# Performance work log

Hardware: AMD Instinct MI355X
Metric: run time of the kernel (lower is better)

The kernel has to match this reference:

```python
import jax, jax.numpy as jnp
import numpy as np

WL_IDX = 0          # water_level_index
THRESH = 0.1        # anomaly threshold
B, T, I, H, O = 2048, 2048, 8, 24, 1


def setup_inputs() -> dict:
    key = jax.random.key(0)
    ks = jax.random.split(key, 7)
    s = float(1.0 / np.sqrt(H))  # PyTorch LSTMCell/Linear uniform init bound
    x = jax.random.normal(ks[0], (B, T, I), dtype=jnp.float32)
    W_ih = jax.random.uniform(ks[1], (4 * H, I), minval=-s, maxval=s, dtype=jnp.float32)
    W_hh = jax.random.uniform(ks[2], (4 * H, H), minval=-s, maxval=s, dtype=jnp.float32)
    b_ih = jax.random.uniform(ks[3], (4 * H,), minval=-s, maxval=s, dtype=jnp.float32)
    b_hh = jax.random.uniform(ks[4], (4 * H,), minval=-s, maxval=s, dtype=jnp.float32)
    W_out = jax.random.uniform(ks[5], (O, H), minval=-s, maxval=s, dtype=jnp.float32)
    b_out = jax.random.uniform(ks[6], (O,), minval=-s, maxval=s, dtype=jnp.float32)
    return {"x": x, "W_ih": W_ih, "W_hh": W_hh, "b_ih": b_ih, "b_hh": b_hh,
            "W_out": W_out, "b_out": b_out}


def reference(x, W_ih, W_hh, b_ih, b_hh, W_out, b_out):
    # x: (B, T, I) -> preds: (B, T, O)
    Bs, Ts, Is = x.shape
    Hs = W_hh.shape[1]
    h0 = jnp.zeros((Bs, Hs), x.dtype)
    c0 = jnp.zeros((Bs, Hs), x.dtype)
    # Init pred equal to t=0 water level -> anomaly flag is False at t=0,
    # reproducing the original's ungated first step.
    pred0 = x[:, 0, WL_IDX:WL_IDX + 1]  # (B, 1)
    xs = jnp.swapaxes(x, 0, 1)  # (T, B, I)

    def step(carry, x_t):
        h, c, pred = carry
        actual = x_t[:, WL_IDX:WL_IDX + 1]            # (B, 1)
        anom = jnp.abs(pred - actual) > THRESH         # (B, 1) bool
        wl = jnp.where(anom[:, 0], pred[:, 0], x_t[:, WL_IDX])
        inp = x_t.at[:, WL_IDX].set(wl)                # anomaly-gated input
        # LSTMCell: gates in PyTorch order i, f, g, o
        gates = inp @ W_ih.T + b_ih + h @ W_hh.T + b_hh  # (B, 4H)
        i_g, f_g, g_g, o_g = jnp.split(gates, 4, axis=1)
        c_new = jax.nn.sigmoid(f_g) * c + jax.nn.sigmoid(i_g) * jnp.tanh(g_g)
        h_new = jax.nn.sigmoid(o_g) * jnp.tanh(c_new)
        pred_new = h_new @ W_out.T + b_out             # (B, O)
        return (h_new, c_new, pred_new), pred_new

    _, preds = jax.lax.scan(step, (h0, c0, pred0), xs)  # (T, B, O)
    return jnp.swapaxes(preds, 0, 1)  # (B, T, O)
```

## Files before the change

kernel.cpp:

```cpp
#include <hip/hip_runtime.h>

#define TT 2048
#define II 8
#define HH 24
#define THRESH 0.1f
#define LOG2E 1.4426950408889634f

typedef float v2f __attribute__((ext_vector_type(2)));

#define ROR_ADD(a, N)                                                          \
    {                                                                          \
        int t_ = __builtin_amdgcn_update_dpp(0, __float_as_int(a),             \
                                             0x120 + (N), 0xF, 0xF, false);    \
        (a) += __int_as_float(t_);                                             \
    }

__global__ __launch_bounds__(64)
__attribute__((amdgpu_waves_per_eu(2, 2)))
void lstm_anom_kernel(const float* __restrict__ x,
                      const float* __restrict__ W_ih,
                      const float* __restrict__ W_hh,
                      const float* __restrict__ b_ih,
                      const float* __restrict__ b_hh,
                      const float* __restrict__ W_out,
                      const float* __restrict__ b_out,
                      float* __restrict__ out)
{
    __shared__ __align__(16) float vbuf[32];

    const int  lane  = threadIdx.x;
    const int  b     = blockIdx.x;
    const int  l32   = lane & 31;
    const bool hi    = lane >= 32;
    const bool unitL = (l32 < HH);
    const int  jc    = unitL ? l32 : 0;
    const bool xL    = (!hi) && (l32 >= 24);
    const int  xk    = l32 - 24;

    const float* xb = x + (size_t)b * (TT * II);

    const int rowA = (hi ? 2 * HH : 0) + jc;
    const int rowB = rowA + HH;
    volatile const float* vW_ih = W_ih;
    volatile const float* vW_hh = W_hh;

    v2f wA2[16], wB2[16];
    #pragma unroll
    for (int k = 0; k < 4; ++k) {
        wA2[k] = (v2f){ vW_ih[rowA * II + 2 * k], vW_ih[rowA * II + 2 * k + 1] };
        wB2[k] = (v2f){ vW_ih[rowB * II + 2 * k], vW_ih[rowB * II + 2 * k + 1] };
    }
    #pragma unroll
    for (int k = 0; k < 12; ++k) {
        wA2[4 + k] = (v2f){ vW_hh[rowA * HH + 2 * k], vW_hh[rowA * HH + 2 * k + 1] };
        wB2[4 + k] = (v2f){ vW_hh[rowB * HH + 2 * k], vW_hh[rowB * HH + 2 * k + 1] };
    }
    const float biasA = b_ih[rowA] + b_hh[rowA];
    const float biasB = b_ih[rowB] + b_hh[rowB];
    const float kA = hi ? (-2.f * LOG2E) : (-LOG2E);
    const float mA = hi ? 2.f : 1.f;
    const float nA = hi ? -1.f : 0.f;
    const float woutj = unitL ? W_out[jc] : 0.f;
    const float bout  = b_out[0];

    if (lane < 32) vbuf[lane] = (lane < 8) ? xb[lane] : 0.f;
    float xA = 0.f, xB = 0.f;
    if (xL) xA = xb[II + xk];
    __syncthreads();

    v2f v2r[16];
    #pragma unroll
    for (int c8 = 0; c8 < 8; ++c8) {
        const float4 q = *(const float4*)&vbuf[c8 * 4];
        v2r[c8 * 2]     = (v2f){q.x, q.y};
        v2r[c8 * 2 + 1] = (v2f){q.z, q.w};
    }
    float pred = v2r[0].x;
    float cst = 0.f, predsave = 0.f;

    for (int t = 0; t < TT; ++t) {
        v2r[0].x = (fabsf(pred - v2r[0].x) > THRESH) ? pred : v2r[0].x;

        v2f accA = (v2f){biasA, 0.f};
        v2f accB = (v2f){biasB, 0.f};
        #pragma unroll
        for (int k = 0; k < 16; ++k) {
            accA = __builtin_elementwise_fma(wA2[k], v2r[k], accA);
            accB = __builtin_elementwise_fma(wB2[k], v2r[k], accB);
        }
        const float aA = accA.x + accA.y;
        const float aB = accB.x + accB.y;

        const float sA = __builtin_amdgcn_rcpf(1.f + __builtin_amdgcn_exp2f(kA * aA));
        const float tA = fmaf(sA, mA, nA);
        const float sB = __builtin_amdgcn_rcpf(1.f + __builtin_amdgcn_exp2f(-LOG2E * aB));
        auto rA = __builtin_amdgcn_permlane32_swap(__float_as_int(tA), __float_as_int(tA), false, false);
        auto rB = __builtin_amdgcn_permlane32_swap(__float_as_int(sB), __float_as_int(sB), false, false);
        const float ig = __int_as_float(rA[0]);
        const float gg = __int_as_float(rA[1]);
        const float fg = __int_as_float(rB[0]);
        const float og = __int_as_float(rB[1]);

        cst = fmaf(fg, cst, ig * gg);
        const float sc = __builtin_amdgcn_rcpf(1.f + __builtin_amdgcn_exp2f(-2.f * LOG2E * cst));
        const float tc = fmaf(2.f, sc, -1.f);
        const float h  = og * tc;

        if (lane < 32) vbuf[xL ? xk : (8 + l32)] = xL ? xA : h;
        if (xL) {
            int tn = t + 2; if (tn > TT - 1) tn = TT - 1;
            xB = xb[(size_t)tn * II + xk];
        }

        float p = woutj * h;
        {
            auto r = __builtin_amdgcn_permlane16_swap(__float_as_int(p), __float_as_int(p), false, false);
            p = __int_as_float(r[0]) + __int_as_float(r[1]);
        }
        ROR_ADD(p, 8); ROR_ADD(p, 4); ROR_ADD(p, 2); ROR_ADD(p, 1);
        pred = p + bout;

        predsave = ((t & 63) == lane) ? pred : predsave;
        if ((t & 63) == 63) out[(size_t)b * TT + (t - 63) + lane] = predsave;

        #pragma unroll
        for (int c8 = 0; c8 < 8; ++c8) {
            const float4 q = *(const float4*)&vbuf[c8 * 4];
            v2r[c8 * 2]     = (v2f){q.x, q.y};
            v2r[c8 * 2 + 1] = (v2f){q.z, q.w};
        }
        if (xL) xA = xB;
    }
}

extern "C" void kernel_launch(void* const* d_in, const int* in_sizes, int n_in,
                              void* d_out, int out_size, void* d_ws, size_t ws_size,
                              hipStream_t stream) {
    const float* x     = (const float*)d_in[0];
    const float* W_ih  = (const float*)d_in[1];
    const float* W_hh  = (const float*)d_in[2];
    const float* b_ih  = (const float*)d_in[3];
    const float* b_hh  = (const float*)d_in[4];
    const float* W_out = (const float*)d_in[5];
    const float* b_out = (const float*)d_in[6];
    float* out = (float*)d_out;

    dim3 grid(2048);
    dim3 block(64);
    lstm_anom_kernel<<<grid, block, 0, stream>>>(x, W_ih, W_hh, b_ih, b_hh,
                                                 W_out, b_out, out);
}
```

Measured before the change: 749.4 us.

## Fold output projection into gate matvec via spare lane and readlane

Spare lane 24 now carries W_out as its weight row, so the prediction for step t-1 comes out of the same FMA chain that builds the gate pre-activations and is broadcast with readlane. This removes the per-step permlane16 swap and four-stage DPP reduction for the output dot product. The anomaly gate on x[0] is now applied after the matvec as a correction term (w0*v0), which takes the gating off the start of the critical path. Costs include an extra readlane dependency ahead of the activations, x-prefetch lanes moved to 25-28 in both halves, an epilogue to emit the final prediction, and weight loads changed from volatile scalar to float4.

Measured after the change: 724.4 us. 1.03x faster.

```diff
diff --git a/kernel.cpp b/kernel.cpp
--- a/kernel.cpp
+++ b/kernel.cpp
@@ -8,12 +8,9 @@
 
 typedef float v2f __attribute__((ext_vector_type(2)));
 
-#define ROR_ADD(a, N)                                                          \
-    {                                                                          \
-        int t_ = __builtin_amdgcn_update_dpp(0, __float_as_int(a),             \
-                                             0x120 + (N), 0xF, 0xF, false);    \
-        (a) += __int_as_float(t_);                                             \
-    }
+__device__ __forceinline__ float readlane_f(float v, int l) {
+    return __int_as_float(__builtin_amdgcn_readlane(__float_as_int(v), l));
+}
 
 __global__ __launch_bounds__(64)
 __attribute__((amdgpu_waves_per_eu(2, 2)))
@@ -32,40 +29,54 @@
     const int  b     = blockIdx.x;
     const int  l32   = lane & 31;
     const bool hi    = lane >= 32;
-    const bool unitL = (l32 < HH);
-    const int  jc    = unitL ? l32 : 0;
-    const bool xL    = (!hi) && (l32 >= 24);
-    const int  xk    = l32 - 24;
+    const int  jc    = (l32 < HH) ? l32 : 0;
+    const bool xLn   = (l32 >= 25 && l32 <= 28);
+    const int  xk    = (l32 - 25) + (hi ? 4 : 0);
 
     const float* xb = x + (size_t)b * (TT * II);
 
     const int rowA = (hi ? 2 * HH : 0) + jc;
     const int rowB = rowA + HH;
-    volatile const float* vW_ih = W_ih;
-    volatile const float* vW_hh = W_hh;
-
+    float wAf[32], wBf[32];
+    #pragma unroll
+    for (int q = 0; q < 2; ++q) {
+        const float4 qa = *(const float4*)(W_ih + rowA * II + q * 4);
+        const float4 qb = *(const float4*)(W_ih + rowB * II + q * 4);
+        wAf[q*4+0]=qa.x; wAf[q*4+1]=qa.y; wAf[q*4+2]=qa.z; wAf[q*4+3]=qa.w;
+        wBf[q*4+0]=qb.x; wBf[q*4+1]=qb.y; wBf[q*4+2]=qb.z; wBf[q*4+3]=qb.w;
+    }
+    #pragma unroll
+    for (int q = 0; q < 6; ++q) {
+        const float4 qa = *(const float4*)(W_hh + rowA * HH + q * 4);
+        const float4 qb = *(const float4*)(W_hh + rowB * HH + q * 4);
+        wAf[8+q*4+0]=qa.x; wAf[8+q*4+1]=qa.y; wAf[8+q*4+2]=qa.z; wAf[8+q*4+3]=qa.w;
+        wBf[8+q*4+0]=qb.x; wBf[8+q*4+1]=qb.y; wBf[8+q*4+2]=qb.z; wBf[8+q*4+3]=qb.w;
+    }
+    float biasA = b_ih[rowA] + b_hh[rowA];
+    float biasB = b_ih[rowB] + b_hh[rowB];
+    const float bout = b_out[0];
+    float w0A = wAf[0], w0B = wBf[0];
+    wAf[0] = 0.f; wBf[0] = 0.f;
+    if (lane == 24) {
+        #pragma unroll
+        for (int k = 0; k < 32; ++k) { wAf[k] = 0.f; wBf[k] = 0.f; }
+        #pragma unroll
+        for (int j = 0; j < HH; ++j) wAf[8 + j] = W_out[j];
+        biasA = bout; biasB = 0.f; w0A = 0.f; w0B = 0.f;
+    }
     v2f wA2[16], wB2[16];
     #pragma unroll
-    for (int k = 0; k < 4; ++k) {
-        wA2[k] = (v2f){ vW_ih[rowA * II + 2 * k], vW_ih[rowA * II + 2 * k + 1] };
-        wB2[k] = (v2f){ vW_ih[rowB * II + 2 * k], vW_ih[rowB * II + 2 * k + 1] };
+    for (int k = 0; k < 16; ++k) {
+        wA2[k] = (v2f){ wAf[2*k], wAf[2*k+1] };
+        wB2[k] = (v2f){ wBf[2*k], wBf[2*k+1] };
     }
-    #pragma unroll
-    for (int k = 0; k < 12; ++k) {
-        wA2[4 + k] = (v2f){ vW_hh[rowA * HH + 2 * k], vW_hh[rowA * HH + 2 * k + 1] };
-        wB2[4 + k] = (v2f){ vW_hh[rowB * HH + 2 * k], vW_hh[rowB * HH + 2 * k + 1] };
-    }
-    const float biasA = b_ih[rowA] + b_hh[rowA];
-    const float biasB = b_ih[rowB] + b_hh[rowB];
     const float kA = hi ? (-2.f * LOG2E) : (-LOG2E);
     const float mA = hi ? 2.f : 1.f;
     const float nA = hi ? -1.f : 0.f;
-    const float woutj = unitL ? W_out[jc] : 0.f;
-    const float bout  = b_out[0];
 
     if (lane < 32) vbuf[lane] = (lane < 8) ? xb[lane] : 0.f;
     float xA = 0.f, xB = 0.f;
-    if (xL) xA = xb[II + xk];
+    if (xLn) xA = xb[II + xk];
     __syncthreads();
 
     v2f v2r[16];
@@ -75,12 +86,9 @@
         v2r[c8 * 2]     = (v2f){q.x, q.y};
         v2r[c8 * 2 + 1] = (v2f){q.z, q.w};
     }
-    float pred = v2r[0].x;
     float cst = 0.f, predsave = 0.f;
 
     for (int t = 0; t < TT; ++t) {
-        v2r[0].x = (fabsf(pred - v2r[0].x) > THRESH) ? pred : v2r[0].x;
-
         v2f accA = (v2f){biasA, 0.f};
         v2f accB = (v2f){biasB, 0.f};
         #pragma unroll
@@ -88,8 +96,15 @@
             accA = __builtin_elementwise_fma(wA2[k], v2r[k], accA);
             accB = __builtin_elementwise_fma(wB2[k], v2r[k], accB);
         }
-        const float aA = accA.x + accA.y;
-        const float aB = accB.x + accB.y;
+        float aA = accA.x + accA.y;
+        float aB = accB.x + accB.y;
+
+        const float x0    = v2r[0].x;
+        const float predR = readlane_f(aA, 24);
+        const float predS = (t == 0) ? x0 : predR;
+        const float v0    = (fabsf(predS - x0) > THRESH) ? predS : x0;
+        aA = fmaf(w0A, v0, aA);
+        aB = fmaf(w0B, v0, aB);
 
         const float sA = __builtin_amdgcn_rcpf(1.f + __builtin_amdgcn_exp2f(kA * aA));
         const float tA = fmaf(sA, mA, nA);
@@ -106,22 +121,14 @@
         const float tc = fmaf(2.f, sc, -1.f);
         const float h  = og * tc;
 
-        if (lane < 32) vbuf[xL ? xk : (8 + l32)] = xL ? xA : h;
-        if (xL) {
+        predsave = (((t - 1) & 63) == lane) ? predS : predsave;
+        if (t && (t & 63) == 0) out[(size_t)b * TT + (t - 64) + lane] = predsave;
+
+        if (lane < HH || xLn) vbuf[xLn ? xk : (8 + l32)] = xLn ? xA : h;
+        if (xLn) {
             int tn = t + 2; if (tn > TT - 1) tn = TT - 1;
             xB = xb[(size_t)tn * II + xk];
         }
-
-        float p = woutj * h;
-        {
-            auto r = __builtin_amdgcn_permlane16_swap(__float_as_int(p), __float_as_int(p), false, false);
-            p = __int_as_float(r[0]) + __int_as_float(r[1]);
-        }
-        ROR_ADD(p, 8); ROR_ADD(p, 4); ROR_ADD(p, 2); ROR_ADD(p, 1);
-        pred = p + bout;
-
-        predsave = ((t & 63) == lane) ? pred : predsave;
-        if ((t & 63) == 63) out[(size_t)b * TT + (t - 63) + lane] = predsave;
 
         #pragma unroll
         for (int c8 = 0; c8 < 8; ++c8) {
@@ -129,7 +136,17 @@
             v2r[c8 * 2]     = (v2f){q.x, q.y};
             v2r[c8 * 2 + 1] = (v2f){q.z, q.w};
         }
-        if (xL) xA = xB;
+        if (xLn) xA = xB;
+    }
+
+    {
+        v2f accA = (v2f){biasA, 0.f};
+        #pragma unroll
+        for (int k = 0; k < 16; ++k)
+            accA = __builtin_elementwise_fma(wA2[k], v2r[k], accA);
+        const float predL = readlane_f(accA.x + accA.y, 24);
+        predsave = (lane == 63) ? predL : predsave;
+        out[(size_t)b * TT + (TT - 64) + lane] = predsave;
     }
 }
 
```
